# Kernel optimization log

Hardware: AMD Instinct MI355X
Metric: run time of the kernel (lower is better)

The kernel has to match this reference:

```python
import jax, jax.numpy as jnp
import numpy as np

B, C, T, F = 2, 1, 8640, 8
HID = 16
MIN_H, MAX_H = 4.0, 48.0
SAMPLES_PER_HOUR = 60.0 * 6.0  # 10-second sampling


def setup_inputs() -> dict:
    key = jax.random.key(0)
    k1, k2, k3, k4 = jax.random.split(key, 4)
    attenuation = jax.random.normal(k1, (B, C, T), dtype=jnp.float32) * 2.0 + 10.0
    metadata = jax.random.normal(k2, (B, F), dtype=jnp.float32)
    # window-predictor MLP params (Linear(F,16) -> ReLU -> Linear(16,1) -> Sigmoid)
    w1 = jax.random.normal(k3, (F, HID), dtype=jnp.float32) * 0.35
    b1 = jnp.zeros((HID,), jnp.float32)
    w2 = jax.random.normal(k4, (HID, 1), dtype=jnp.float32) * 0.25
    b2 = jnp.zeros((1,), jnp.float32)
    return {"attenuation": attenuation, "metadata": metadata,
            "w1": w1, "b1": b1, "w2": w2, "b2": b2}


def _max_window(metadata, w1, b1, w2, b2, time_samples):
    # Mirrors the torch window predictor; result is a concrete Python int
    # (torch uses .item(), so the window size is a shape, not a traced value).
    h = jax.nn.relu(metadata @ w1 + b1)
    factor = jax.nn.sigmoid(h @ w2 + b2)[:, 0]            # [B]
    hours = MIN_H + factor * (MAX_H - MIN_H)
    samples = (hours * SAMPLES_PER_HOUR).astype(jnp.int32)  # .long() truncation
    return min(int(jnp.max(samples)), time_samples)


def reference(attenuation, metadata, w1, b1, w2, b2):
    t = attenuation.shape[2]
    max_window = _max_window(metadata, w1, b1, w2, b2, t)
    pad = max_window // 2
    midx = (max_window - 1) // 2  # torch.median picks the LOWER middle element
    # replicate padding == torch 'replicate'
    x = jnp.pad(attenuation, ((0, 0), (0, 0), (pad, pad)), mode="edge")
    n_out = x.shape[2] - max_window + 1  # unfold count with step=1
    # sliding windows via gather: [B, C, n_out, W]
    idx = jnp.arange(n_out)[:, None] + jnp.arange(max_window)[None, :]
    windows = x[:, :, idx]
    # median over window dim (lower-middle element, matching torch.median)
    return jnp.sort(windows, axis=-1)[..., midx]
```

## Files before the change

kernel.cpp:

```cpp
#include <hip/hip_runtime.h>
#include <math.h>


__device__ __forceinline__ int bin_of(float x, float vmin, float scale, int NB) {
    int v = (int)((x - vmin) * scale);
    return v < 0 ? 0 : (v > NB - 1 ? NB - 1 : v);
}

__global__ void __launch_bounds__(256) k_setup(
    const float* __restrict__ atten, const float* __restrict__ md,
    const float* __restrict__ w1, const float* __restrict__ b1,
    const float* __restrict__ w2, const float* __restrict__ b2,
    int* __restrict__ hdr_i, float* __restrict__ hdr_f,
    int T, int n_out, int nTot)
{
    __shared__ float smin[4], smax[4];
    int tid = threadIdx.x;
    int strideS = nTot >> 10; if (strideS < 1) strideS = 1;
    float vmin = 3.0e38f, vmax = -3.0e38f;
    #pragma unroll
    for (int q = 0; q < 4; ++q) {
        int idx = (tid + q * 256) * strideS;
        if (idx < nTot) {
            float x = atten[idx];
            vmin = fminf(vmin, x); vmax = fmaxf(vmax, x);
        }
    }
    #pragma unroll
    for (int off = 1; off < 64; off <<= 1) {
        vmin = fminf(vmin, __shfl_xor(vmin, off));
        vmax = fmaxf(vmax, __shfl_xor(vmax, off));
    }
    if ((tid & 63) == 0) { smin[tid >> 6] = vmin; smax[tid >> 6] = vmax; }
    __syncthreads();
    if (tid < 64) {
        int lane = tid;
        float m1 = (lane < 4) ? smin[lane] : 3.0e38f;
        float m2 = (lane < 4) ? smax[lane] : -3.0e38f;
        #pragma unroll
        for (int off = 1; off < 4; off <<= 1) {
            m1 = fminf(m1, __shfl_xor(m1, off));
            m2 = fmaxf(m2, __shfl_xor(m2, off));
        }
        int samples = 0;
        if (lane < 32) {
            int b = lane >> 4, j = lane & 15;
            float acc = b1[j];
            #pragma unroll
            for (int f = 0; f < 8; ++f) acc += md[b * 8 + f] * w1[f * 16 + j];
            float h = fmaxf(acc, 0.0f);
            float p = h * w2[j];
            #pragma unroll
            for (int off = 1; off < 16; off <<= 1) p += __shfl_xor(p, off);
            float s = p + b2[0];
            float factor = 1.0f / (1.0f + expf(-s));
            float hours = 4.0f + factor * (48.0f - 4.0f);
            samples = (int)(hours * 360.0f);
        }
        #pragma unroll
        for (int off = 1; off < 64; off <<= 1) samples = max(samples, __shfl_xor(samples, off));
        int mw = min(samples, T);
        int want_even = (n_out == T + 1) ? 1 : 0;
        if ((((mw & 1) == 0) ? 1 : 0) != want_even) { if (mw < T) mw += 1; else mw -= 1; }
        if (mw < 1) mw = 1;
        if (lane == 0) {
            hdr_i[0] = mw;
            hdr_i[1] = mw >> 1;
            hdr_i[2] = (mw - 1) >> 1;
            hdr_f[3] = m1;
            hdr_f[4] = m2;
        }
    }
}

template<int NB>
__global__ void __launch_bounds__(256) k_hist(
    const float* __restrict__ atten, unsigned char* __restrict__ binIdx,
    unsigned short* __restrict__ tileCnt, const float* __restrict__ hdr_f,
    int T, int NTe)
{
    __shared__ unsigned int hist[4][NB];
    int wave = threadIdx.x >> 6;
    int lane = threadIdx.x & 63;
    int g = blockIdx.x * 4 + wave;
    bool valid = g < 2 * NTe;
    int b = g / NTe, tile = g - b * NTe;

    #pragma unroll
    for (int j = lane; j < NB; j += 64) hist[wave][j] = 0;
    __syncthreads();

    int t = tile * 64 + lane;
    if (valid && t < T) {
        float vmin = hdr_f[3], vmax = hdr_f[4];
        float scale = (float)NB / fmaxf(vmax - vmin, 1e-10f);
        float x = atten[(size_t)b * T + t];
        int v = bin_of(x, vmin, scale, NB);
        binIdx[(size_t)b * T + t] = (unsigned char)v;
        atomicAdd(&hist[wave][v], 1u);
    }
    __syncthreads();
    if (valid) {
        unsigned short* row = tileCnt + ((size_t)b * NTe + tile) * NB;
        #pragma unroll
        for (int j = lane; j < NB; j += 64) row[j] = (unsigned short)hist[wave][j];
    }
}

template<int NB>
__global__ void __launch_bounds__(64) k_cdf_scatter(
    const unsigned char* __restrict__ binIdx, const unsigned short* __restrict__ tileCnt,
    const float* __restrict__ atten,
    unsigned short* __restrict__ F, float* __restrict__ bval,
    int T, int NTe, int NTr16)
{
    constexpr int VPL = NB / 64;
    int blk = blockIdx.x;
    int b = blk / NTr16, r = blk - b * NTr16;
    int lane = threadIdx.x;
    int v0 = lane * VPL;
    int t0 = r * 16;
    int eb = t0 >> 6;
    int lead = t0 & 63;

    int bs[VPL], ts[VPL];
    if (VPL == 4) {
        const uint2* cb2 = (const uint2*)(tileCnt + (size_t)b * NTe * NB) + lane;
        const int stride = NB / 4;
        unsigned bax[8], bay[8], tax[8], tay[8];
        #pragma unroll
        for (int q = 0; q < 8; ++q) { bax[q] = bay[q] = tax[q] = tay[q] = 0u; }
        int rp = 0;
        for (; rp + 8 <= NTe; rp += 8) {
            #pragma unroll
            for (int q = 0; q < 8; ++q) {
                uint2 u = cb2[(size_t)(rp + q) * stride];
                bool inb = (rp + q) < eb;
                tax[q] += u.x; tay[q] += u.y;
                bax[q] += inb ? u.x : 0u; bay[q] += inb ? u.y : 0u;
            }
        }
        for (; rp < NTe; ++rp) {
            uint2 u = cb2[(size_t)rp * stride];
            bool inb = rp < eb;
            tax[0] += u.x; tay[0] += u.y;
            bax[0] += inb ? u.x : 0u; bay[0] += inb ? u.y : 0u;
        }
        unsigned bsx = 0, bsy = 0, tsx = 0, tsy = 0;
        #pragma unroll
        for (int q = 0; q < 8; ++q) { bsx += bax[q]; bsy += bay[q]; tsx += tax[q]; tsy += tay[q]; }
        bs[0] = (int)(bsx & 0xFFFFu); bs[1] = (int)(bsx >> 16);
        bs[2] = (int)(bsy & 0xFFFFu); bs[VPL - 1] = (int)(bsy >> 16);
        ts[0] = (int)(tsx & 0xFFFFu); ts[1] = (int)(tsx >> 16);
        ts[2] = (int)(tsy & 0xFFFFu); ts[VPL - 1] = (int)(tsy >> 16);
    } else {
        const unsigned short* cb = tileCnt + (size_t)b * NTe * NB + v0;
        int ba[8], taq[8];
        #pragma unroll
        for (int q = 0; q < 8; ++q) { ba[q] = 0; taq[q] = 0; }
        int rp = 0;
        for (; rp + 8 <= NTe; rp += 8) {
            #pragma unroll
            for (int q = 0; q < 8; ++q) {
                int u = (int)cb[(size_t)(rp + q) * NB];
                taq[q] += u;
                ba[q] += ((rp + q) < eb) ? u : 0;
            }
        }
        for (; rp < NTe; ++rp) {
            int u = (int)cb[(size_t)rp * NB];
            taq[0] += u;
            ba[0] += (rp < eb) ? u : 0;
        }
        #pragma unroll
        for (int q = 1; q < 8; ++q) { ba[0] += ba[q]; taq[0] += taq[q]; }
        bs[0] = ba[0]; ts[0] = taq[0];
    }

    int c[VPL], totI[VPL];
    {
        int loc = 0;
        #pragma unroll
        for (int kk = 0; kk < VPL; ++kk) { loc += bs[kk]; c[kk] = loc; }
        int incl = loc;
        #pragma unroll
        for (int off = 1; off < 64; off <<= 1) {
            int n = __shfl_up(incl, off);
            if (lane >= off) incl += n;
        }
        int excl = incl - loc;
        #pragma unroll
        for (int kk = 0; kk < VPL; ++kk) c[kk] += excl;
    }
    {
        int loc = 0;
        #pragma unroll
        for (int kk = 0; kk < VPL; ++kk) { loc += ts[kk]; totI[kk] = loc; }
        int incl = loc;
        #pragma unroll
        for (int off = 1; off < 64; off <<= 1) {
            int n = __shfl_up(incl, off);
            if (lane >= off) incl += n;
        }
        int excl = incl - loc;
        #pragma unroll
        for (int kk = 0; kk < VPL; ++kk) totI[kk] += excl;
    }
    int totLeft = __shfl_up(totI[VPL - 1], 1);
    if (lane == 0) totLeft = 0;

    const unsigned char* bi = binIdx + (size_t)b * T;

    int myLead = (lane < lead && (eb * 64 + lane) < T) ? (int)bi[eb * 64 + lane] : 0;
    for (int j = 0; j < lead; ++j) {
        int bt = __shfl(myLead, j);
        #pragma unroll
        for (int kk = 0; kk < VPL; ++kk) c[kk] += (v0 + kk >= bt) ? 1 : 0;
    }

    int t1 = min(T + 1, t0 + 16);
    bool has16 = (lane < 16) && (t0 + lane) < T;
    int   myb = has16 ? (int)bi[t0 + lane] : 0;
    float myx = has16 ? atten[(size_t)b * T + t0 + lane] : 0.0f;
    unsigned short* Fb = F + (size_t)b * (T + 1) * NB;
    float* bvb = bval + (size_t)b * T;
    for (int t = t0; t < t1; ++t) {
        unsigned short* Ft = Fb + (size_t)t * NB + v0;
        if (VPL == 4) {
            uint2 pk;
            pk.x = (unsigned)c[0] | ((unsigned)c[1] << 16);
            pk.y = (unsigned)c[2] | ((unsigned)c[VPL - 1] << 16);
            *(uint2*)Ft = pk;
        } else {
            Ft[0] = (unsigned short)c[0];
        }
        if (t < T) {
            int j = t - t0;
            int bt = __shfl(myb, j);
            float xv = __shfl(myx, j);
            int cLeft = __shfl_up(c[VPL - 1], 1);
            if (lane == 0) cLeft = 0;
            int ow  = (VPL == 4) ? (bt >> 2) : bt;
            int lc  = (VPL == 4) ? (bt & 3) : 0;
            if (lane == ow) {
                int prevc   = lc ? c[lc - 1]    : cLeft;
                int within  = c[lc] - prevc;
                int prevTot = lc ? totI[lc - 1] : totLeft;
                bvb[prevTot + within] = xv;
            }
            #pragma unroll
            for (int kk = 0; kk < VPL; ++kk) c[kk] += (v0 + kk >= bt) ? 1 : 0;
        }
    }
}

template<int NB>
__global__ void __launch_bounds__(256) k_query(
    const float* __restrict__ atten, const unsigned short* __restrict__ F,
    const float* __restrict__ bval,
    const int* __restrict__ hdr_i, const float* __restrict__ hdr_f,
    float* __restrict__ out, int T, int n_out)
{
    constexpr int VPL = NB / 64;
    int wid = (blockIdx.x * 256 + threadIdx.x) >> 6;
    int lane = threadIdx.x & 63;
    if (wid >= 2 * n_out) return;
    int b = wid / n_out, o = wid - b * n_out;

    int mw = hdr_i[0], pad = hdr_i[1], k = hdr_i[2];
    float vmin = hdr_f[3], vmax = hdr_f[4];
    float scale = (float)NB / fmaxf(vmax - vmin, 1e-10f);

    int lo_t = o - pad;
    int ta = max(lo_t, 0);
    int tb = min(lo_t + mw, T);
    int L  = ta - lo_t;
    int Rr = lo_t + mw - tb;

    const float* xb = atten + (size_t)b * T;
    float x0 = xb[0], xT = xb[T - 1];
    int b0 = bin_of(x0, vmin, scale, NB);
    int bT = bin_of(xT, vmin, scale, NB);

    const unsigned short* Fb = F + (size_t)b * (T + 1) * NB;
    int fa[VPL], fb[VPL];
    {
        const unsigned short* pa = Fb + (size_t)ta * NB + lane * VPL;
        const unsigned short* pb = Fb + (size_t)tb * NB + lane * VPL;
        if (VPL == 4) {
            uint2 ua = *(const uint2*)pa;
            fa[0] = (int)(ua.x & 0xFFFFu); fa[1] = (int)(ua.x >> 16);
            fa[2] = (int)(ua.y & 0xFFFFu); fa[VPL - 1] = (int)(ua.y >> 16);
            uint2 ub = *(const uint2*)pb;
            fb[0] = (int)(ub.x & 0xFFFFu); fb[1] = (int)(ub.x >> 16);
            fb[2] = (int)(ub.y & 0xFFFFu); fb[VPL - 1] = (int)(ub.y >> 16);
        } else {
            fa[0] = (int)pa[0]; fb[0] = (int)pb[0];
        }
    }

    int kk = k + 1;
    int w[VPL];
    #pragma unroll
    for (int j = 0; j < VPL; ++j) {
        int v = lane * VPL + j;
        w[j] = fb[j] - fa[j] + (b0 <= v ? L : 0) + (bT <= v ? Rr : 0);
    }
    unsigned long long m = __ballot(w[VPL - 1] >= kk);
    int ll = (int)__ffsll(m) - 1;

    int wj[VPL], faj[VPL], fbj[VPL];
    #pragma unroll
    for (int j = 0; j < VPL; ++j) {
        wj[j]  = __shfl(w[j], ll);
        faj[j] = __shfl(fa[j], ll);
        fbj[j] = __shfl(fb[j], ll);
    }
    int wprevL  = __shfl(w[VPL - 1], ll - 1);
    int faPrevL = __shfl(fa[VPL - 1], ll - 1);
    int fbPrevL = __shfl(fb[VPL - 1], ll - 1);
    if (ll == 0) { wprevL = 0; faPrevL = 0; fbPrevL = 0; }

    int jj = VPL - 1;
    #pragma unroll
    for (int j = VPL - 1; j >= 0; --j) if (wj[j] >= kk) jj = j;
    int bsel = ll * VPL + jj;
    int wprev = jj > 0 ? wj[jj - 1] : wprevL;
    int faSel = faj[jj], fbSel = fbj[jj];
    int pA = jj > 0 ? faj[jj - 1] : faPrevL;
    int pB = jj > 0 ? fbj[jj - 1] : fbPrevL;

    int kp = k - wprev;
    int withinA = faSel - pA;
    int cntw = (fbSel - pB) - withinA;
    int s0 = bsel ? (int)Fb[(size_t)T * NB + bsel - 1] : 0;
    int j0 = s0 + withinA;
    int j1e = j0 + cntw;

    int Lc = (b0 == bsel) ? L : 0;
    int Rc = (bT == bsel) ? Rr : 0;

    const float* bv = bval + (size_t)b * T;

    const int CAND = 4;
    float rr[CAND];
    bool reg = (cntw <= 64 * CAND);
    float cmin = 3.0e38f, cmax = -3.0e38f;
    if (reg) {
        #pragma unroll
        for (int q = 0; q < CAND; ++q) {
            int idx = j0 + lane + q * 64;
            if (idx < j1e) {
                float v = bv[idx];
                rr[q] = v;
                cmin = fminf(cmin, v); cmax = fmaxf(cmax, v);
            } else {
                rr[q] = 3.0e38f;
            }
        }
    } else {
        for (int j = j0 + lane; j < j1e; j += 64) {
            float v = bv[j];
            cmin = fminf(cmin, v); cmax = fmaxf(cmax, v);
        }
    }
    #pragma unroll
    for (int off = 1; off < 64; off <<= 1) {
        cmin = fminf(cmin, __shfl_xor(cmin, off));
        cmax = fmaxf(cmax, __shfl_xor(cmax, off));
    }
    if (Lc > 0) { cmin = fminf(cmin, x0); cmax = fmaxf(cmax, x0); }
    if (Rc > 0) { cmin = fminf(cmin, xT); cmax = fmaxf(cmax, xT); }

    float vlo = cmin, vhi = cmax;
    int need = kp + 1;
    for (int it = 0; it < 20; ++it) {
        float vm = 0.5f * (vlo + vhi);
        int cnt = ((x0 < vm) ? Lc : 0) + ((xT < vm) ? Rc : 0);
        if (reg) {
            #pragma unroll
            for (int q = 0; q < CAND; ++q)
                cnt += __popcll(__ballot(rr[q] < vm));
        } else {
            int my = 0;
            for (int j = j0 + lane; j < j1e; j += 64) my += (bv[j] < vm) ? 1 : 0;
            #pragma unroll
            for (int off = 1; off < 64; off <<= 1) my += __shfl_xor(my, off);
            cnt += my;
        }
        if (cnt >= need) vhi = vm; else vlo = vm;
    }
    if (lane == 0) out[(size_t)b * n_out + o] = 0.5f * (vlo + vhi);
}

__global__ void __launch_bounds__(256) k_fallback(
    const float* __restrict__ atten, const int* __restrict__ hdr_i,
    float* __restrict__ out, int T, int n_out)
{
    int wave = threadIdx.x >> 6;
    int lane = threadIdx.x & 63;
    int gid = blockIdx.x * 4 + wave;
    if (gid >= 2 * n_out) return;
    int b = gid / n_out;
    int o = gid - b * n_out;
    int mw = hdr_i[0], pad = hdr_i[1], k = hdr_i[2];
    const float* xb = atten + (size_t)b * T;
    int lo_t = o - pad;
    float lo = 3.0e38f, hi = -3.0e38f;
    for (int i = lane; i < mw; i += 64) {
        int t = lo_t + i;
        t = t < 0 ? 0 : (t >= T ? T - 1 : t);
        float x = xb[t];
        lo = fminf(lo, x); hi = fmaxf(hi, x);
    }
    #pragma unroll
    for (int off = 1; off < 64; off <<= 1) {
        lo = fminf(lo, __shfl_xor(lo, off));
        hi = fmaxf(hi, __shfl_xor(hi, off));
    }
    for (int it = 0; it < 26; ++it) {
        float vm = 0.5f * (lo + hi);
        int c = 0;
        for (int i = lane; i < mw; i += 64) {
            int t = lo_t + i;
            t = t < 0 ? 0 : (t >= T ? T - 1 : t);
            c += (xb[t] < vm) ? 1 : 0;
        }
        #pragma unroll
        for (int off = 1; off < 64; off <<= 1) c += __shfl_xor(c, off);
        if (c >= k + 1) hi = vm; else lo = vm;
    }
    if (lane == 0) out[(size_t)b * n_out + o] = 0.5f * (lo + hi);
}

struct Plan { size_t oBin, oCnt, oF, oV, total; };
static Plan make_plan(int NB, int nTot, int T, int NTe) {
    auto a64 = [](size_t x) { return (x + 63) & ~(size_t)63; };
    Plan p;
    size_t off = 64;
    p.oBin = off; off = a64(off + (size_t)nTot);
    p.oCnt = off; off = a64(off + (size_t)2 * NTe * NB * 2);
    p.oF   = off; off = a64(off + (size_t)2 * (T + 1) * NB * 2);
    p.oV   = off; off = a64(off + (size_t)nTot * 4);
    p.total = off;
    return p;
}

template<int NB>
static void run_pipeline(const float* atten, char* ws, const Plan& p,
                         const int* hdr_i, const float* hdr_f, float* out,
                         int T, int n_out, int nTot, int NTe,
                         hipStream_t stream)
{
    unsigned char*  binIdx  = (unsigned char*)(ws + p.oBin);
    unsigned short* tileCnt = (unsigned short*)(ws + p.oCnt);
    unsigned short* F       = (unsigned short*)(ws + p.oF);
    float*          bval    = (float*)(ws + p.oV);

    int NTr16 = (T + 1 + 15) / 16;
    int histBlocks = (2 * NTe + 3) / 4;
    k_hist<NB><<<dim3(histBlocks), dim3(256), 0, stream>>>(atten, binIdx, tileCnt, hdr_f, T, NTe);
    k_cdf_scatter<NB><<<dim3(2 * NTr16), dim3(64), 0, stream>>>(binIdx, tileCnt, atten, F, bval, T, NTe, NTr16);
    int nWaves = 2 * n_out;
    k_query<NB><<<dim3((nWaves + 3) / 4), dim3(256), 0, stream>>>(atten, F, bval, hdr_i, hdr_f, out, T, n_out);
}

extern "C" void kernel_launch(void* const* d_in, const int* in_sizes, int n_in,
                              void* d_out, int out_size, void* d_ws, size_t ws_size,
                              hipStream_t stream)
{
    const float* atten = (const float*)d_in[0];
    const float* md    = (const float*)d_in[1];
    const float* w1    = (const float*)d_in[2];
    const float* b1    = (const float*)d_in[3];
    const float* w2    = (const float*)d_in[4];
    const float* b2    = (const float*)d_in[5];
    float* out = (float*)d_out;

    const int B = 2;
    const int nTot  = in_sizes[0];
    const int T     = nTot / B;
    const int n_out = out_size / B;
    const int NTe = (T + 63) / 64;

    char* ws = (char*)d_ws;
    int*   hdr_i = (int*)ws;
    float* hdr_f = (float*)ws;

    k_setup<<<dim3(1), dim3(256), 0, stream>>>(atten, md, w1, b1, w2, b2,
                                               hdr_i, hdr_f, T, n_out, nTot);

    Plan p256 = make_plan(256, nTot, T, NTe);
    Plan p64  = make_plan(64,  nTot, T, NTe);
    if (ws_size >= p256.total) {
        run_pipeline<256>(atten, ws, p256, hdr_i, hdr_f, out, T, n_out, nTot, NTe, stream);
    } else if (ws_size >= p64.total) {
        run_pipeline<64>(atten, ws, p64, hdr_i, hdr_f, out, T, n_out, nTot, NTe, stream);
    } else {
        int blocks = (2 * n_out + 3) / 4;
        k_fallback<<<dim3(blocks), dim3(256), 0, stream>>>(atten, hdr_i, out, T, n_out);
    }
}
```

Measured before the change: 104.7 us.

## Fold setup kernel into hist and query kernels, cut bisection iterations

Removes the single-block k_setup launch by having every k_hist and k_query block recompute the sampled min/max and the MLP-derived window size redundantly. This saves one kernel launch and its serial dependency, at the cost of each block doing extra global loads. It also removes the per-wave __syncthreads around the histogram, which relies on each wave only touching its own shared row. The bisection iterations in k_query drop from 20 to 14, which lowers output precision and risks tolerance failures.

```diff
diff --git a/kernel.cpp b/kernel.cpp
--- a/kernel.cpp
+++ b/kernel.cpp
@@ -7,103 +7,65 @@
     return v < 0 ? 0 : (v > NB - 1 ? NB - 1 : v);
 }
 
-__global__ void __launch_bounds__(256) k_setup(
-    const float* __restrict__ atten, const float* __restrict__ md,
-    const float* __restrict__ w1, const float* __restrict__ b1,
-    const float* __restrict__ w2, const float* __restrict__ b2,
-    int* __restrict__ hdr_i, float* __restrict__ hdr_f,
-    int T, int n_out, int nTot)
-{
-    __shared__ float smin[4], smax[4];
+__device__ __forceinline__ void sampled_minmax_256(
+    const float* __restrict__ atten, int nTot, float* sred ,
+    float& m1, float& m2)
+{
     int tid = threadIdx.x;
+    int wave = tid >> 6, lane = tid & 63;
     int strideS = nTot >> 10; if (strideS < 1) strideS = 1;
-    float vmin = 3.0e38f, vmax = -3.0e38f;
+    float vmn = 3.0e38f, vmx = -3.0e38f;
     #pragma unroll
     for (int q = 0; q < 4; ++q) {
         int idx = (tid + q * 256) * strideS;
         if (idx < nTot) {
             float x = atten[idx];
-            vmin = fminf(vmin, x); vmax = fmaxf(vmax, x);
+            vmn = fminf(vmn, x); vmx = fmaxf(vmx, x);
         }
     }
     #pragma unroll
     for (int off = 1; off < 64; off <<= 1) {
-        vmin = fminf(vmin, __shfl_xor(vmin, off));
-        vmax = fmaxf(vmax, __shfl_xor(vmax, off));
-    }
-    if ((tid & 63) == 0) { smin[tid >> 6] = vmin; smax[tid >> 6] = vmax; }
+        vmn = fminf(vmn, __shfl_xor(vmn, off));
+        vmx = fmaxf(vmx, __shfl_xor(vmx, off));
+    }
+    if (lane == 0) { sred[wave] = vmn; sred[4 + wave] = vmx; }
     __syncthreads();
-    if (tid < 64) {
-        int lane = tid;
-        float m1 = (lane < 4) ? smin[lane] : 3.0e38f;
-        float m2 = (lane < 4) ? smax[lane] : -3.0e38f;
-        #pragma unroll
-        for (int off = 1; off < 4; off <<= 1) {
-            m1 = fminf(m1, __shfl_xor(m1, off));
-            m2 = fmaxf(m2, __shfl_xor(m2, off));
-        }
-        int samples = 0;
-        if (lane < 32) {
-            int b = lane >> 4, j = lane & 15;
-            float acc = b1[j];
-            #pragma unroll
-            for (int f = 0; f < 8; ++f) acc += md[b * 8 + f] * w1[f * 16 + j];
-            float h = fmaxf(acc, 0.0f);
-            float p = h * w2[j];
-            #pragma unroll
-            for (int off = 1; off < 16; off <<= 1) p += __shfl_xor(p, off);
-            float s = p + b2[0];
-            float factor = 1.0f / (1.0f + expf(-s));
-            float hours = 4.0f + factor * (48.0f - 4.0f);
-            samples = (int)(hours * 360.0f);
-        }
-        #pragma unroll
-        for (int off = 1; off < 64; off <<= 1) samples = max(samples, __shfl_xor(samples, off));
-        int mw = min(samples, T);
-        int want_even = (n_out == T + 1) ? 1 : 0;
-        if ((((mw & 1) == 0) ? 1 : 0) != want_even) { if (mw < T) mw += 1; else mw -= 1; }
-        if (mw < 1) mw = 1;
-        if (lane == 0) {
-            hdr_i[0] = mw;
-            hdr_i[1] = mw >> 1;
-            hdr_i[2] = (mw - 1) >> 1;
-            hdr_f[3] = m1;
-            hdr_f[4] = m2;
-        }
-    }
+    m1 = fminf(fminf(sred[0], sred[1]), fminf(sred[2], sred[3]));
+    m2 = fmaxf(fmaxf(sred[4], sred[5]), fmaxf(sred[6], sred[7]));
 }
 
 template<int NB>
 __global__ void __launch_bounds__(256) k_hist(
     const float* __restrict__ atten, unsigned char* __restrict__ binIdx,
-    unsigned short* __restrict__ tileCnt, const float* __restrict__ hdr_f,
-    int T, int NTe)
+    unsigned short* __restrict__ tileCnt, int T, int NTe, int nTot)
 {
     __shared__ unsigned int hist[4][NB];
+    __shared__ float sred[8];
+    float m1, m2;
+    sampled_minmax_256(atten, nTot, sred, m1, m2);
+    float scale = (float)NB / fmaxf(m2 - m1, 1e-10f);
+
     int wave = threadIdx.x >> 6;
     int lane = threadIdx.x & 63;
     int g = blockIdx.x * 4 + wave;
     bool valid = g < 2 * NTe;
     int b = g / NTe, tile = g - b * NTe;
 
-    #pragma unroll
-    for (int j = lane; j < NB; j += 64) hist[wave][j] = 0;
-    __syncthreads();
+    unsigned int* h = hist[wave];
+    #pragma unroll
+    for (int j = lane; j < NB; j += 64) h[j] = 0u;
 
     int t = tile * 64 + lane;
     if (valid && t < T) {
-        float vmin = hdr_f[3], vmax = hdr_f[4];
-        float scale = (float)NB / fmaxf(vmax - vmin, 1e-10f);
         float x = atten[(size_t)b * T + t];
-        int v = bin_of(x, vmin, scale, NB);
+        int v = bin_of(x, m1, scale, NB);
         binIdx[(size_t)b * T + t] = (unsigned char)v;
-        atomicAdd(&hist[wave][v], 1u);
-    }
-    __syncthreads();
+        atomicAdd(&h[v], 1u);
+    }
     if (valid) {
         unsigned short* row = tileCnt + ((size_t)b * NTe + tile) * NB;
         #pragma unroll
-        for (int j = lane; j < NB; j += 64) row[j] = (unsigned short)hist[wave][j];
+        for (int j = lane; j < NB; j += 64) row[j] = (unsigned short)h[j];
     }
 }
 
@@ -258,18 +220,53 @@
 __global__ void __launch_bounds__(256) k_query(
     const float* __restrict__ atten, const unsigned short* __restrict__ F,
     const float* __restrict__ bval,
-    const int* __restrict__ hdr_i, const float* __restrict__ hdr_f,
-    float* __restrict__ out, int T, int n_out)
+    const float* __restrict__ md, const float* __restrict__ w1,
+    const float* __restrict__ b1, const float* __restrict__ w2,
+    const float* __restrict__ b2,
+    float* __restrict__ out, int T, int n_out, int nTot)
 {
     constexpr int VPL = NB / 64;
-    int wid = (blockIdx.x * 256 + threadIdx.x) >> 6;
-    int lane = threadIdx.x & 63;
+    __shared__ float sred[8];
+    __shared__ int   smwi[3];
+    int tid = threadIdx.x;
+    int lane = tid & 63;
+
+    float m1, m2;
+    sampled_minmax_256(atten, nTot, sred, m1, m2);
+
+    if (tid < 64) {
+        int samples = 0;
+        if (lane < 32) {
+            int b = lane >> 4, j = lane & 15;
+            float acc = b1[j];
+            #pragma unroll
+            for (int f = 0; f < 8; ++f) acc += md[b * 8 + f] * w1[f * 16 + j];
+            float h = fmaxf(acc, 0.0f);
+            float p = h * w2[j];
+            #pragma unroll
+            for (int off = 1; off < 16; off <<= 1) p += __shfl_xor(p, off);
+            float s = p + b2[0];
+            float factor = 1.0f / (1.0f + expf(-s));
+            float hours = 4.0f + factor * (48.0f - 4.0f);
+            samples = (int)(hours * 360.0f);
+        }
+        #pragma unroll
+        for (int off = 1; off < 64; off <<= 1) samples = max(samples, __shfl_xor(samples, off));
+        int mw = min(samples, T);
+        int want_even = (n_out == T + 1) ? 1 : 0;
+        if ((((mw & 1) == 0) ? 1 : 0) != want_even) { if (mw < T) mw += 1; else mw -= 1; }
+        if (mw < 1) mw = 1;
+        if (lane == 0) { smwi[0] = mw; smwi[1] = mw >> 1; smwi[2] = (mw - 1) >> 1; }
+    }
+    __syncthreads();
+
+    const int mw = smwi[0], pad = smwi[1], k = smwi[2];
+    const float vmin = m1;
+    const float scale = (float)NB / fmaxf(m2 - m1, 1e-10f);
+
+    int wid = (blockIdx.x * 256 + tid) >> 6;
     if (wid >= 2 * n_out) return;
     int b = wid / n_out, o = wid - b * n_out;
-
-    int mw = hdr_i[0], pad = hdr_i[1], k = hdr_i[2];
-    float vmin = hdr_f[3], vmax = hdr_f[4];
-    float scale = (float)NB / fmaxf(vmax - vmin, 1e-10f);
 
     int lo_t = o - pad;
     int ta = max(lo_t, 0);
@@ -374,7 +371,7 @@
 
     float vlo = cmin, vhi = cmax;
     int need = kp + 1;
-    for (int it = 0; it < 20; ++it) {
+    for (int it = 0; it < 14; ++it) {
         float vm = 0.5f * (vlo + vhi);
         int cnt = ((x0 < vm) ? Lc : 0) + ((xT < vm) ? Rc : 0);
         if (reg) {
@@ -394,16 +391,47 @@
 }
 
 __global__ void __launch_bounds__(256) k_fallback(
-    const float* __restrict__ atten, const int* __restrict__ hdr_i,
+    const float* __restrict__ atten,
+    const float* __restrict__ md, const float* __restrict__ w1,
+    const float* __restrict__ b1, const float* __restrict__ w2,
+    const float* __restrict__ b2,
     float* __restrict__ out, int T, int n_out)
 {
-    int wave = threadIdx.x >> 6;
-    int lane = threadIdx.x & 63;
+    __shared__ int smwi[3];
+    int tid = threadIdx.x;
+    int wave = tid >> 6;
+    int lane = tid & 63;
+    if (tid < 64) {
+        int samples = 0;
+        if (lane < 32) {
+            int b = lane >> 4, j = lane & 15;
+            float acc = b1[j];
+            #pragma unroll
+            for (int f = 0; f < 8; ++f) acc += md[b * 8 + f] * w1[f * 16 + j];
+            float h = fmaxf(acc, 0.0f);
+            float p = h * w2[j];
+            #pragma unroll
+            for (int off = 1; off < 16; off <<= 1) p += __shfl_xor(p, off);
+            float s = p + b2[0];
+            float factor = 1.0f / (1.0f + expf(-s));
+            float hours = 4.0f + factor * (48.0f - 4.0f);
+            samples = (int)(hours * 360.0f);
+        }
+        #pragma unroll
+        for (int off = 1; off < 64; off <<= 1) samples = max(samples, __shfl_xor(samples, off));
+        int mw = min(samples, T);
+        int want_even = (n_out == T + 1) ? 1 : 0;
+        if ((((mw & 1) == 0) ? 1 : 0) != want_even) { if (mw < T) mw += 1; else mw -= 1; }
+        if (mw < 1) mw = 1;
+        if (lane == 0) { smwi[0] = mw; smwi[1] = mw >> 1; smwi[2] = (mw - 1) >> 1; }
+    }
+    __syncthreads();
+    int mw = smwi[0], pad = smwi[1], k = smwi[2];
+
     int gid = blockIdx.x * 4 + wave;
     if (gid >= 2 * n_out) return;
     int b = gid / n_out;
     int o = gid - b * n_out;
-    int mw = hdr_i[0], pad = hdr_i[1], k = hdr_i[2];
     const float* xb = atten + (size_t)b * T;
     int lo_t = o - pad;
     float lo = 3.0e38f, hi = -3.0e38f;
@@ -447,8 +475,10 @@
 }
 
 template<int NB>
-static void run_pipeline(const float* atten, char* ws, const Plan& p,
-                         const int* hdr_i, const float* hdr_f, float* out,
+static void run_pipeline(const float* atten, const float* md,
+                         const float* w1, const float* b1,
+                         const float* w2, const float* b2,
+                         char* ws, const Plan& p, float* out,
                          int T, int n_out, int nTot, int NTe,
                          hipStream_t stream)
 {
@@ -456,13 +486,16 @@
     unsigned short* tileCnt = (unsigned short*)(ws + p.oCnt);
     unsigned short* F       = (unsigned short*)(ws + p.oF);
     float*          bval    = (float*)(ws + p.oV);
-
     int NTr16 = (T + 1 + 15) / 16;
+
     int histBlocks = (2 * NTe + 3) / 4;
-    k_hist<NB><<<dim3(histBlocks), dim3(256), 0, stream>>>(atten, binIdx, tileCnt, hdr_f, T, NTe);
-    k_cdf_scatter<NB><<<dim3(2 * NTr16), dim3(64), 0, stream>>>(binIdx, tileCnt, atten, F, bval, T, NTe, NTr16);
+    k_hist<NB><<<dim3(histBlocks), dim3(256), 0, stream>>>(
+        atten, binIdx, tileCnt, T, NTe, nTot);
+    k_cdf_scatter<NB><<<dim3(2 * NTr16), dim3(64), 0, stream>>>(
+        binIdx, tileCnt, atten, F, bval, T, NTe, NTr16);
     int nWaves = 2 * n_out;
-    k_query<NB><<<dim3((nWaves + 3) / 4), dim3(256), 0, stream>>>(atten, F, bval, hdr_i, hdr_f, out, T, n_out);
+    k_query<NB><<<dim3((nWaves + 3) / 4), dim3(256), 0, stream>>>(
+        atten, F, bval, md, w1, b1, w2, b2, out, T, n_out, nTot);
 }
 
 extern "C" void kernel_launch(void* const* d_in, const int* in_sizes, int n_in,
@@ -484,20 +517,18 @@
     const int NTe = (T + 63) / 64;
 
     char* ws = (char*)d_ws;
-    int*   hdr_i = (int*)ws;
-    float* hdr_f = (float*)ws;
-
-    k_setup<<<dim3(1), dim3(256), 0, stream>>>(atten, md, w1, b1, w2, b2,
-                                               hdr_i, hdr_f, T, n_out, nTot);
 
     Plan p256 = make_plan(256, nTot, T, NTe);
     Plan p64  = make_plan(64,  nTot, T, NTe);
     if (ws_size >= p256.total) {
-        run_pipeline<256>(atten, ws, p256, hdr_i, hdr_f, out, T, n_out, nTot, NTe, stream);
+        run_pipeline<256>(atten, md, w1, b1, w2, b2, ws, p256, out,
+                          T, n_out, nTot, NTe, stream);
     } else if (ws_size >= p64.total) {
-        run_pipeline<64>(atten, ws, p64, hdr_i, hdr_f, out, T, n_out, nTot, NTe, stream);
+        run_pipeline<64>(atten, md, w1, b1, w2, b2, ws, p64, out,
+                         T, n_out, nTot, NTe, stream);
     } else {
         int blocks = (2 * n_out + 3) / 4;
-        k_fallback<<<dim3(blocks), dim3(256), 0, stream>>>(atten, hdr_i, out, T, n_out);
-    }
-}
+        k_fallback<<<dim3(blocks), dim3(256), 0, stream>>>(
+            atten, md, w1, b1, w2, b2, out, T, n_out);
+    }
+}
```

Measured after the change: 109.4 us. 4.5% more time.
